# Kernel tuning notes

Hardware: AMD Instinct MI355X
Metric: run time of the kernel (lower is better)

Reference implementation:

```python
import jax, jax.numpy as jnp
import numpy as np

B, L1, LQ, LA, H = 32, 512, 32, 32, 128  # dialog turns, doc len, q len, a len, hidden
NEG = -1e30  # finite stand-in for torch's -inf (avoids NaN for fully-masked row 0, which is dropped by zero_first anyway)


def setup_inputs() -> dict:
    key = jax.random.key(0)
    ks = jax.random.split(key, 6)
    return {
        "xd_emb": jax.random.normal(ks[0], (B, L1, H), jnp.float32),
        "xq_emb": jax.random.normal(ks[1], (B, LQ, H), jnp.float32),
        "xa_emb": jax.random.normal(ks[2], (B, LA, H), jnp.float32),
        "W": jax.random.normal(ks[3], (H, H), jnp.float32) / np.sqrt(H).astype(np.float32),
        "b": jnp.zeros((H,), jnp.float32),
        "recency_weight": jnp.full((1,), -0.5, jnp.float32),
        "xq_mask": jax.random.randint(ks[4], (B, LQ), 0, 2).astype(bool),
        "xa_mask": jax.random.randint(ks[5], (B, LA), 0, 2).astype(bool),
    }


def _forward(xd_emb, xq_emb, xa_emb, W, b, recency_weight, xq_mask, xa_mask):
    Bn = xq_emb.shape[0]
    M = xq_emb.shape[1] + xa_emb.shape[1]  # max_dialog_len (max_qa_len)
    dlg = jnp.concatenate([xq_emb, xa_emb], axis=1).reshape(Bn * M, -1)  # (B*M, h) flattened dialog
    pad_mask = jnp.concatenate([xq_mask, xa_mask], axis=1).reshape(-1)    # (B*M,)

    ts = jnp.arange(Bn)
    j_ts = jnp.arange(Bn * M) // M  # timestep of each flattened dialog token
    # triu(ones, k=0) repeated M times along cols: timestep i masks tokens of timesteps >= i
    causal = j_ts[None, :] >= ts[:, None]            # (B, B*M)
    y_mask = causal | pad_mask[None, :]              # (B, B*M), True = masked

    # Linear + ReLU projections; y_proj computed once (no explicit (B, B*M, h) tiling)
    x_proj = jax.nn.relu(xd_emb @ W.T + b)           # (B, L1, h)
    y_proj = jax.nn.relu(dlg @ W.T + b)              # (B*M, h)

    scores = jnp.einsum('bld,kd->blk', x_proj, y_proj)      # (B, L1, B*M)
    scores = jnp.where(y_mask[:, None, :], jnp.float32(NEG), scores)

    # toeplitz recency bias: |i - j_ts| * recency_weight, row 0 zeroed (zero_first)
    rw = recency_weight[0] * jnp.abs(ts[:, None] - j_ts[None, :]).astype(jnp.float32)
    rw = jnp.concatenate([jnp.zeros_like(rw[:1]), rw[1:]], axis=0)
    scores = scores + rw[:, None, :]

    alpha = jax.nn.softmax(scores, axis=-1)
    alpha = jnp.concatenate([jnp.zeros_like(alpha[:1]), alpha[1:]], axis=0)  # zero_first
    return jnp.einsum('blk,kd->bld', alpha, dlg)     # weighted sum over original (unprojected) dialog


def reference(xd_emb, xq_emb, xa_emb, W, b, recency_weight, xq_mask, xa_mask):
    return _forward(xd_emb, xq_emb, xa_emb, W, b, recency_weight, xq_mask, xa_mask)
```

## Files before the change

### kernel.cpp

```cpp
#include <hip/hip_runtime.h>
#include <stdint.h>

#define NEGV (-1e30f)

constexpr int L1_ = 512;
constexpr int H_  = 128;
constexpr int NK_ = 2048;

typedef __attribute__((ext_vector_type(8))) _Float16 f16x8;
typedef __attribute__((ext_vector_type(2))) __fp16   h16x2;
typedef __attribute__((ext_vector_type(4))) float    f32x4;

static __device__ __forceinline__ uint16_t f2h(float x) {
    union { _Float16 h; uint16_t u; } cv; cv.h = (_Float16)x; return cv.u;
}


__global__ __launch_bounds__(256) void preproc_kernel(
        const float* __restrict__ xq,
        const float* __restrict__ xa,
        const float* __restrict__ W,
        const float* __restrict__ bias,
        const uint8_t* __restrict__ qm,
        const uint8_t* __restrict__ am,
        uint8_t* __restrict__ Y2,
        uint8_t* __restrict__ V2,
        uint8_t* __restrict__ W2,
        float* __restrict__ badd) {
    int b = blockIdx.x;
    int tid = threadIdx.x;
    __shared__ __align__(16) float sbuf[64 * 128];

    if (b < 128) {
        int k0 = b * 16;
        f32x4* xr4 = (f32x4*)sbuf;
#pragma unroll
        for (int i = 0; i < 2; ++i) {
            int idx = tid + i * 256;
            int row = idx >> 5, d4 = idx & 31;
            int k = k0 + row;
            int b2 = k >> 6, r = k & 63;
            const float* src = (r < 32) ? (xq + (size_t)(b2 * 32 + r) * H_)
                                        : (xa + (size_t)(b2 * 32 + (r - 32)) * H_);
            xr4[idx] = *(const f32x4*)(src + d4 * 4);
        }
        __syncthreads();
        int c = tid & 127, rh = tid >> 7;
        float acc[8];
#pragma unroll
        for (int i = 0; i < 8; ++i) acc[i] = 0.0f;
        const f32x4* w4 = (const f32x4*)(W + (size_t)c * H_);
        for (int d4 = 0; d4 < 32; ++d4) {
            f32x4 wv = w4[d4];
#pragma unroll
            for (int i = 0; i < 8; ++i) {
                f32x4 x = xr4[(rh * 8 + i) * 32 + d4];
                acc[i] += wv[0]*x[0] + wv[1]*x[1] + wv[2]*x[2] + wv[3]*x[3];
            }
        }
        float bc = bias[c];
        float* res = sbuf + 2048;
#pragma unroll
        for (int i = 0; i < 8; ++i)
            res[(rh * 8 + i) * H_ + c] = fmaxf(acc[i] + bc, 0.0f);
        __syncthreads();
        int ks = tid >> 6, l = tid & 63, n16 = l & 15, g = l >> 4;
        uint16_t hbuf[8];
#pragma unroll
        for (int j = 0; j < 8; ++j)
            hbuf[j] = f2h(res[n16 * H_ + ks * 32 + g * 8 + j]);
        uint8_t* dst = Y2 + (((size_t)b * 4 + ks) << 10) + l * 16;
        *(uint64_t*)dst       = ((const uint64_t*)hbuf)[0];
        *(uint64_t*)(dst + 8) = ((const uint64_t*)hbuf)[1];
    } else if (b < 160) {
        int kt = b - 128;
        f32x4* ld4 = (f32x4*)sbuf;
#pragma unroll
        for (int i = 0; i < 8; ++i) {
            int idx = tid + i * 256;
            int row = idx >> 5, d4 = idx & 31;
            const float* src = (row < 32) ? (xq + (size_t)(kt * 32 + row) * H_)
                                          : (xa + (size_t)(kt * 32 + row - 32) * H_);
            ld4[idx] = *(const f32x4*)(src + d4 * 4);
        }
        __syncthreads();
#pragma unroll
        for (int i = 0; i < 4; ++i) {
            int id = tid + i * 256;
            int cT = id >> 7, ks = (id >> 6) & 1, l = id & 63;
            int n16 = l & 15, g = l >> 4;
            uint16_t hbuf[8];
#pragma unroll
            for (int j = 0; j < 8; ++j)
                hbuf[j] = f2h(sbuf[(ks * 32 + g * 8 + j) * H_ + cT * 16 + n16]);
            uint8_t* dst = V2 + (((size_t)kt * 16 + cT * 2 + ks) << 10) + l * 16;
            *(uint64_t*)dst       = ((const uint64_t*)hbuf)[0];
            *(uint64_t*)(dst + 8) = ((const uint64_t*)hbuf)[1];
        }
    } else if (b == 160) {
        int* flags = (int*)sbuf;
        if (tid == 0) { flags[0] = 0; flags[1] = 0; }
        __syncthreads();
        uint32_t v = ((const uint32_t*)qm)[tid] | ((const uint32_t*)am)[tid];
        if (v & 0xFFu)        atomicOr(&flags[0], 1);
        if (v & 0xFFFFFF00u)  atomicOr(&flags[1], 1);
        __syncthreads();
        int f0 = flags[0], f1 = flags[1];
        int mode = (f0 && !f1) ? 0 : ((!f0 && f1) ? 1 : 2);
        for (int k = tid; k < NK_; k += 256) {
            int b2 = k >> 6, r = k & 63;
            int idx = b2 * 32 + (r < 32 ? r : r - 32);
            const uint8_t* src = (r < 32) ? qm : am;
            int p;
            if (mode == 0)      p = (((const int*)src)[idx] != 0);
            else if (mode == 1) p = (((const float*)src)[idx] != 0.0f);
            else                p = (src[idx] != 0);
            badd[k] = p ? NEGV : 0.0f;
        }
    } else {
        for (int h = 0; h < 2; ++h) {
            f32x4* s4 = (f32x4*)sbuf;
#pragma unroll
            for (int i = 0; i < 8; ++i) {
                int idx = tid + i * 256;
                s4[idx] = *(const f32x4*)(W + (size_t)h * 64 * H_ + idx * 4);
            }
            __syncthreads();
#pragma unroll
            for (int i = 0; i < 4; ++i) {
                int id = tid + i * 256;
                int ct = id >> 8, ks = (id >> 6) & 3, l = id & 63;
                int n16 = l & 15, g = l >> 4;
                uint16_t hb[8];
#pragma unroll
                for (int j = 0; j < 8; ++j)
                    hb[j] = f2h(sbuf[(ct * 16 + n16) * H_ + ks * 32 + g * 8 + j]);
                uint8_t* dst = W2 + (((size_t)((h * 4 + ct) * 4 + ks)) << 10) + l * 16;
                *(uint64_t*)dst       = ((const uint64_t*)hb)[0];
                *(uint64_t*)(dst + 8) = ((const uint64_t*)hb)[1];
            }
            __syncthreads();
        }
    }
}

__global__ __launch_bounds__(256, 2) void attn_kernel(
        const float*   __restrict__ xd,
        const uint8_t* __restrict__ W2,
        const float*   __restrict__ bias,
        const uint8_t* __restrict__ Y2,
        const uint8_t* __restrict__ V2,
        const float*   __restrict__ badd,
        const float*   __restrict__ rw,
        float* __restrict__ out) {
    int bid = blockIdx.x;
    int t, lt;
    if (bid < 256) { int p = bid >> 4; t = (p < 15) ? 31 - p : 16; lt = bid & 15; }
    else           { int b2 = bid - 256; int p = b2 >> 4; t = (p < 15) ? p + 1 : 0; lt = b2 & 15; }
    int l0 = lt << 5;
    int tid = threadIdx.x;

    __shared__ __align__(16) float smem[4 * 64 * 64];
    __shared__ float stats_m[4][32];
    __shared__ float stats_l[4][32];

    if (t == 0) {
        f32x4 z = {0.f, 0.f, 0.f, 0.f};
        f32x4* o4 = (f32x4*)(out + (size_t)l0 * H_);
        for (int i = tid; i < 32 * H_ / 4; i += 256) o4[i] = z;
        return;
    }

    int w = tid >> 6, lane = tid & 63, n16 = lane & 15, g = lane >> 4;
    int prow0 = n16, prow1 = 16 + n16;
    int swzP = (n16 & 7) << 4;

    uint16_t* xbuf  = (uint16_t*)((char*)smem + 16384);
    uint16_t* xpbuf = (uint16_t*)((char*)smem + 24576);
    {
        const float* xsrc = xd + (size_t)(t * L1_ + l0) * H_;
#pragma unroll
        for (int i = 0; i < 4; ++i) {
            int idx = tid + i * 256;
            int row = idx >> 5, c4 = idx & 31;
            f32x4 v = *(const f32x4*)(xsrc + idx * 4);
            uint16_t hb[4] = { f2h(v[0]), f2h(v[1]), f2h(v[2]), f2h(v[3]) };
            *(uint64_t*)((char*)xbuf + row * 256 + ((c4 * 8) ^ ((row & 7) << 4)))
                = *(const uint64_t*)hb;
        }
    }
    __syncthreads();
    {
        f16x8 af[2][4];
#pragma unroll
        for (int rT = 0; rT < 2; ++rT) {
            int row = rT * 16 + n16, swz = (row & 7) << 4;
#pragma unroll
            for (int ks = 0; ks < 4; ++ks)
                af[rT][ks] = *(const f16x8*)((char*)xbuf + row * 256 + ((ks * 64 + g * 16) ^ swz));
        }
        int cTa = 2 * w, cTb = 2 * w + 1;
        f32x4 z4 = {0.f, 0.f, 0.f, 0.f};
        f32x4 d00 = z4, d01 = z4, d10 = z4, d11 = z4;
#pragma unroll
        for (int ks = 0; ks < 4; ++ks) {
            f16x8 wfa = *(const f16x8*)(W2 + (((size_t)cTa * 4 + ks) << 10) + lane * 16);
            f16x8 wfb = *(const f16x8*)(W2 + (((size_t)cTb * 4 + ks) << 10) + lane * 16);
            d00 = __builtin_amdgcn_mfma_f32_16x16x32_f16(af[0][ks], wfa, d00, 0, 0, 0);
            d10 = __builtin_amdgcn_mfma_f32_16x16x32_f16(af[1][ks], wfa, d10, 0, 0, 0);
            d01 = __builtin_amdgcn_mfma_f32_16x16x32_f16(af[0][ks], wfb, d01, 0, 0, 0);
            d11 = __builtin_amdgcn_mfma_f32_16x16x32_f16(af[1][ks], wfb, d11, 0, 0, 0);
        }
        float bba = bias[cTa * 16 + n16], bbb = bias[cTb * 16 + n16];
#pragma unroll
        for (int rT = 0; rT < 2; ++rT) {
            const f32x4& da = rT ? d10 : d00;
            const f32x4& db = rT ? d11 : d01;
#pragma unroll
            for (int q = 0; q < 4; ++q) {
                int row = rT * 16 + g * 4 + q, swz = (row & 7) << 4;
                *(uint16_t*)((char*)xpbuf + row * 256 + (((cTa * 16 + n16) * 2) ^ swz))
                    = f2h(fmaxf(da[q] + bba, 0.0f));
                *(uint16_t*)((char*)xpbuf + row * 256 + (((cTb * 16 + n16) * 2) ^ swz))
                    = f2h(fmaxf(db[q] + bbb, 0.0f));
            }
        }
    }
    __syncthreads();
    f16x8 xf[2][4];
#pragma unroll
    for (int rT = 0; rT < 2; ++rT) {
        int row = rT * 16 + n16, swz = (row & 7) << 4;
#pragma unroll
        for (int ks = 0; ks < 4; ++ks)
            xf[rT][ks] = *(const f16x8*)((char*)xpbuf + row * 256 + ((ks * 64 + g * 16) ^ swz));
    }

    f32x4 zero4 = {0.f, 0.f, 0.f, 0.f};
    f32x4 acc[2][8];
#pragma unroll
    for (int a = 0; a < 2; ++a)
#pragma unroll
        for (int c = 0; c < 8; ++c) acc[a][c] = zero4;

    float m_r[2] = {-INFINITY, -INFINITY};
    float l_r[2] = {0.0f, 0.0f};
    float rww = rw[0];

    char* Pw = (char*)smem + w * 4096;

    for (int kt = w; kt < t; kt += 4) {
        const uint8_t* ybase = Y2 + ((size_t)kt << 14) + lane * 16;
        const uint8_t* vbase = V2 + ((size_t)kt << 14) + lane * 16;

        f16x8 yf[4][4];
#pragma unroll
        for (int kkT = 0; kkT < 4; ++kkT)
#pragma unroll
            for (int ks = 0; ks < 4; ++ks)
                yf[kkT][ks] = *(const f16x8*)(ybase + ((kkT * 4 + ks) << 10));
        f16x8 vbA[4][2];
#pragma unroll
        for (int cT = 0; cT < 4; ++cT) {
            vbA[cT][0] = *(const f16x8*)(vbase + ((cT * 2) << 10));
            vbA[cT][1] = *(const f16x8*)(vbase + ((cT * 2 + 1) << 10));
        }
        f32x4 ba4[4];
#pragma unroll
        for (int kkT = 0; kkT < 4; ++kkT)
            ba4[kkT] = *(const f32x4*)(badd + kt * 64 + kkT * 16 + g * 4);
        __builtin_amdgcn_sched_barrier(0);

        f32x4 ss[4][2];
#pragma unroll
        for (int kkT = 0; kkT < 4; ++kkT) { ss[kkT][0] = zero4; ss[kkT][1] = zero4; }
#pragma unroll
        for (int ks = 0; ks < 4; ++ks)
#pragma unroll
            for (int kkT = 0; kkT < 4; ++kkT) {
                ss[kkT][0] = __builtin_amdgcn_mfma_f32_16x16x32_f16(yf[kkT][ks], xf[0][ks], ss[kkT][0], 0, 0, 0);
                ss[kkT][1] = __builtin_amdgcn_mfma_f32_16x16x32_f16(yf[kkT][ks], xf[1][ks], ss[kkT][1], 0, 0, 0);
            }

        f16x8 vbB[4][2];
#pragma unroll
        for (int cT = 0; cT < 4; ++cT) {
            vbB[cT][0] = *(const f16x8*)(vbase + (((cT + 4) * 2) << 10));
            vbB[cT][1] = *(const f16x8*)(vbase + (((cT + 4) * 2 + 1) << 10));
        }
        __builtin_amdgcn_sched_barrier(0);

        float biasK = rww * (float)(t - kt);
#pragma unroll
        for (int kkT = 0; kkT < 4; ++kkT) {
            f32x4 ba = ba4[kkT] + biasK;
            ss[kkT][0] += ba;
            ss[kkT][1] += ba;
        }

        float sc[2];
#pragma unroll
        for (int rT = 0; rT < 2; ++rT) {
            f32x4 mx4 = ss[0][rT];
#pragma unroll
            for (int kkT = 1; kkT < 4; ++kkT) {
                mx4[0] = fmaxf(mx4[0], ss[kkT][rT][0]);
                mx4[1] = fmaxf(mx4[1], ss[kkT][rT][1]);
                mx4[2] = fmaxf(mx4[2], ss[kkT][rT][2]);
                mx4[3] = fmaxf(mx4[3], ss[kkT][rT][3]);
            }
            float mx = fmaxf(fmaxf(mx4[0], mx4[1]), fmaxf(mx4[2], mx4[3]));
            mx = fmaxf(mx, __shfl_xor(mx, 16));
            mx = fmaxf(mx, __shfl_xor(mx, 32));
            float mn = fmaxf(m_r[rT], mx);
            sc[rT] = __expf(m_r[rT] - mn);
            m_r[rT] = mn;
        }

#pragma unroll
        for (int rT = 0; rT < 2; ++rT) {
            int r = rT ? prow1 : prow0;
            float mn = m_r[rT];
            float ps = 0.0f;
#pragma unroll
            for (int kkT = 0; kkT < 4; ++kkT) {
                f32x4 p;
#pragma unroll
                for (int q = 0; q < 4; ++q) p[q] = __expf(ss[kkT][rT][q] - mn);
                ps += (p[0] + p[1]) + (p[2] + p[3]);
                union { h16x2 h2[2]; uint64_t u64; } pk;
                pk.h2[0] = __builtin_amdgcn_cvt_pkrtz(p[0], p[1]);
                pk.h2[1] = __builtin_amdgcn_cvt_pkrtz(p[2], p[3]);
                *(uint64_t*)(Pw + r * 128 + ((kkT * 32 + g * 8) ^ swzP)) = pk.u64;
            }
            ps += __shfl_xor(ps, 16);
            ps += __shfl_xor(ps, 32);
            l_r[rT] = l_r[rT] * sc[rT] + ps;
        }

        asm volatile("s_waitcnt lgkmcnt(0)" ::: "memory");

        if (!__all((sc[0] == 1.0f) && (sc[1] == 1.0f))) {
#pragma unroll
            for (int rT = 0; rT < 2; ++rT) {
                f32x4 s4;
#pragma unroll
                for (int q = 0; q < 4; ++q) s4[q] = __shfl(sc[rT], (g << 2) + q);
#pragma unroll
                for (int cT = 0; cT < 8; ++cT) acc[rT][cT] *= s4;
            }
        }

        f16x8 pa[2][2];
#pragma unroll
        for (int rT = 0; rT < 2; ++rT) {
            int r = rT ? prow1 : prow0;
#pragma unroll
            for (int ks = 0; ks < 2; ++ks)
                pa[rT][ks] = *(const f16x8*)(Pw + r * 128 + ((ks * 64 + g * 16) ^ swzP));
        }
#pragma unroll
        for (int cT = 0; cT < 4; ++cT)
#pragma unroll
            for (int rT = 0; rT < 2; ++rT) {
                acc[rT][cT] = __builtin_amdgcn_mfma_f32_16x16x32_f16(pa[rT][0], vbA[cT][0], acc[rT][cT], 0, 0, 0);
                acc[rT][cT] = __builtin_amdgcn_mfma_f32_16x16x32_f16(pa[rT][1], vbA[cT][1], acc[rT][cT], 0, 0, 0);
            }
#pragma unroll
        for (int cT = 0; cT < 4; ++cT)
#pragma unroll
            for (int rT = 0; rT < 2; ++rT) {
                acc[rT][cT + 4] = __builtin_amdgcn_mfma_f32_16x16x32_f16(pa[rT][0], vbB[cT][0], acc[rT][cT + 4], 0, 0, 0);
                acc[rT][cT + 4] = __builtin_amdgcn_mfma_f32_16x16x32_f16(pa[rT][1], vbB[cT][1], acc[rT][cT + 4], 0, 0, 0);
            }
    }

    if (g == 0) {
        stats_m[w][n16]      = m_r[0];
        stats_m[w][16 + n16] = m_r[1];
        stats_l[w][n16]      = l_r[0];
        stats_l[w][16 + n16] = l_r[1];
    }
    __syncthreads();

    float fac[2][4];
#pragma unroll
    for (int rT = 0; rT < 2; ++rT)
#pragma unroll
        for (int q = 0; q < 4; ++q) {
            int r = rT * 16 + (g << 2) + q;
            float m0 = stats_m[0][r], m1 = stats_m[1][r];
            float m2 = stats_m[2][r], m3 = stats_m[3][r];
            float mf = fmaxf(fmaxf(m0, m1), fmaxf(m2, m3));
            float lf = stats_l[0][r] * __expf(m0 - mf) + stats_l[1][r] * __expf(m1 - mf)
                     + stats_l[2][r] * __expf(m2 - mf) + stats_l[3][r] * __expf(m3 - mf);
            float mw = stats_m[w][r];
            fac[rT][q] = __expf(mw - mf) / lf;
        }

    float* Ob = smem + w * 4096;
#pragma unroll
    for (int rT = 0; rT < 2; ++rT)
#pragma unroll
        for (int cT = 0; cT < 8; ++cT)
#pragma unroll
            for (int q = 0; q < 4; ++q)
                Ob[((rT * 8 + cT) * 4 + q) * 64 + lane] = acc[rT][cT][q] * fac[rT][q];
    __syncthreads();

    size_t obase = (size_t)(t * L1_ + l0) * H_;
#pragma unroll
    for (int s = 0; s < 16; ++s) {
        int slot = w * 16 + s;
        float v = smem[slot * 64 + lane] + smem[4096 + slot * 64 + lane]
                + smem[8192 + slot * 64 + lane] + smem[12288 + slot * 64 + lane];
        int rT = slot >> 5, cT = (slot >> 2) & 7, q = slot & 3;
        out[obase + (size_t)(rT * 16 + (g << 2) + q) * H_ + cT * 16 + n16] = v;
    }
}

extern "C" void kernel_launch(void* const* d_in, const int* in_sizes, int n_in,
                              void* d_out, int out_size, void* d_ws, size_t ws_size,
                              hipStream_t stream) {
    const float*   xd   = (const float*)d_in[0];
    const float*   xq   = (const float*)d_in[1];
    const float*   xa   = (const float*)d_in[2];
    const float*   W    = (const float*)d_in[3];
    const float*   bias = (const float*)d_in[4];
    const float*   rw   = (const float*)d_in[5];
    const uint8_t* qm   = (const uint8_t*)d_in[6];
    const uint8_t* am   = (const uint8_t*)d_in[7];
    float* out = (float*)d_out;

    char* ws = (char*)d_ws;
    float*   badd = (float*)ws;
    uint8_t* Y2   = (uint8_t*)(ws + 8192);
    uint8_t* V2   = (uint8_t*)(ws + 8192 + 524288);
    uint8_t* W2   = (uint8_t*)(ws + 8192 + 2 * 524288);

    preproc_kernel<<<162, 256, 0, stream>>>(xq, xa, W, bias, qm, am,
                                            Y2, V2, W2, badd);
    attn_kernel<<<512, 256, 0, stream>>>(xd, W2, bias, Y2, V2, badd, rw, out);
}
```

Before: 37.14 us.

## Use eight waves per attention block to split key tiles finer

Doubles the attention block from 256 to 512 threads, so eight waves split the key-timestep loop instead of four. Each wave now computes one 16-column slice of the x projection. The cross-wave softmax merge and output reduction cover eight partials, done in two passes over row tiles to fit shared memory. This shortens the serial loop per wave for long timesteps, at the cost of more shared memory, an extra barrier and a larger reduction.

```diff
diff --git a/kernel.cpp b/kernel.cpp
--- a/kernel.cpp
+++ b/kernel.cpp
@@ -144,7 +144,7 @@
     }
 }
 
-__global__ __launch_bounds__(256, 2) void attn_kernel(
+__global__ __launch_bounds__(512, 2) void attn_kernel(
         const float*   __restrict__ xd,
         const uint8_t* __restrict__ W2,
         const float*   __restrict__ bias,
@@ -160,14 +160,14 @@
     int l0 = lt << 5;
     int tid = threadIdx.x;
 
-    __shared__ __align__(16) float smem[4 * 64 * 64];
-    __shared__ float stats_m[4][32];
-    __shared__ float stats_l[4][32];
+    __shared__ __align__(16) float smem[16384];
+    __shared__ float stats_m[8][32];
+    __shared__ float stats_l[8][32];
 
     if (t == 0) {
         f32x4 z = {0.f, 0.f, 0.f, 0.f};
         f32x4* o4 = (f32x4*)(out + (size_t)l0 * H_);
-        for (int i = tid; i < 32 * H_ / 4; i += 256) o4[i] = z;
+        for (int i = tid; i < 32 * H_ / 4; i += 512) o4[i] = z;
         return;
     }
 
@@ -175,13 +175,13 @@
     int prow0 = n16, prow1 = 16 + n16;
     int swzP = (n16 & 7) << 4;
 
-    uint16_t* xbuf  = (uint16_t*)((char*)smem + 16384);
-    uint16_t* xpbuf = (uint16_t*)((char*)smem + 24576);
+    uint16_t* xbuf  = (uint16_t*)((char*)smem + 32768);
+    uint16_t* xpbuf = (uint16_t*)((char*)smem + 40960);
     {
         const float* xsrc = xd + (size_t)(t * L1_ + l0) * H_;
 #pragma unroll
-        for (int i = 0; i < 4; ++i) {
-            int idx = tid + i * 256;
+        for (int i = 0; i < 2; ++i) {
+            int idx = tid + i * 512;
             int row = idx >> 5, c4 = idx & 31;
             f32x4 v = *(const f32x4*)(xsrc + idx * 4);
             uint16_t hb[4] = { f2h(v[0]), f2h(v[1]), f2h(v[2]), f2h(v[3]) };
@@ -199,30 +199,23 @@
             for (int ks = 0; ks < 4; ++ks)
                 af[rT][ks] = *(const f16x8*)((char*)xbuf + row * 256 + ((ks * 64 + g * 16) ^ swz));
         }
-        int cTa = 2 * w, cTb = 2 * w + 1;
         f32x4 z4 = {0.f, 0.f, 0.f, 0.f};
-        f32x4 d00 = z4, d01 = z4, d10 = z4, d11 = z4;
+        f32x4 d0 = z4, d1 = z4;
 #pragma unroll
         for (int ks = 0; ks < 4; ++ks) {
-            f16x8 wfa = *(const f16x8*)(W2 + (((size_t)cTa * 4 + ks) << 10) + lane * 16);
-            f16x8 wfb = *(const f16x8*)(W2 + (((size_t)cTb * 4 + ks) << 10) + lane * 16);
-            d00 = __builtin_amdgcn_mfma_f32_16x16x32_f16(af[0][ks], wfa, d00, 0, 0, 0);
-            d10 = __builtin_amdgcn_mfma_f32_16x16x32_f16(af[1][ks], wfa, d10, 0, 0, 0);
-            d01 = __builtin_amdgcn_mfma_f32_16x16x32_f16(af[0][ks], wfb, d01, 0, 0, 0);
-            d11 = __builtin_amdgcn_mfma_f32_16x16x32_f16(af[1][ks], wfb, d11, 0, 0, 0);
-        }
-        float bba = bias[cTa * 16 + n16], bbb = bias[cTb * 16 + n16];
+            f16x8 wf = *(const f16x8*)(W2 + (((size_t)w * 4 + ks) << 10) + lane * 16);
+            d0 = __builtin_amdgcn_mfma_f32_16x16x32_f16(af[0][ks], wf, d0, 0, 0, 0);
+            d1 = __builtin_amdgcn_mfma_f32_16x16x32_f16(af[1][ks], wf, d1, 0, 0, 0);
+        }
+        float bb = bias[w * 16 + n16];
 #pragma unroll
         for (int rT = 0; rT < 2; ++rT) {
-            const f32x4& da = rT ? d10 : d00;
-            const f32x4& db = rT ? d11 : d01;
+            const f32x4& d = rT ? d1 : d0;
 #pragma unroll
             for (int q = 0; q < 4; ++q) {
                 int row = rT * 16 + g * 4 + q, swz = (row & 7) << 4;
-                *(uint16_t*)((char*)xpbuf + row * 256 + (((cTa * 16 + n16) * 2) ^ swz))
-                    = f2h(fmaxf(da[q] + bba, 0.0f));
-                *(uint16_t*)((char*)xpbuf + row * 256 + (((cTb * 16 + n16) * 2) ^ swz))
-                    = f2h(fmaxf(db[q] + bbb, 0.0f));
+                *(uint16_t*)((char*)xpbuf + row * 256 + (((w * 16 + n16) * 2) ^ swz))
+                    = f2h(fmaxf(d[q] + bb, 0.0f));
             }
         }
     }
@@ -249,7 +242,7 @@
 
     char* Pw = (char*)smem + w * 4096;
 
-    for (int kt = w; kt < t; kt += 4) {
+    for (int kt = w; kt < t; kt += 8) {
         const uint8_t* ybase = Y2 + ((size_t)kt << 14) + lane * 16;
         const uint8_t* vbase = V2 + ((size_t)kt << 14) + lane * 16;
 
@@ -389,33 +382,34 @@
 #pragma unroll
         for (int q = 0; q < 4; ++q) {
             int r = rT * 16 + (g << 2) + q;
-            float m0 = stats_m[0][r], m1 = stats_m[1][r];
-            float m2 = stats_m[2][r], m3 = stats_m[3][r];
-            float mf = fmaxf(fmaxf(m0, m1), fmaxf(m2, m3));
-            float lf = stats_l[0][r] * __expf(m0 - mf) + stats_l[1][r] * __expf(m1 - mf)
-                     + stats_l[2][r] * __expf(m2 - mf) + stats_l[3][r] * __expf(m3 - mf);
-            float mw = stats_m[w][r];
-            fac[rT][q] = __expf(mw - mf) / lf;
-        }
-
-    float* Ob = smem + w * 4096;
-#pragma unroll
-    for (int rT = 0; rT < 2; ++rT)
+            float mf = stats_m[0][r];
+#pragma unroll
+            for (int wv = 1; wv < 8; ++wv) mf = fmaxf(mf, stats_m[wv][r]);
+            float lf = 0.0f;
+#pragma unroll
+            for (int wv = 0; wv < 8; ++wv) lf += stats_l[wv][r] * __expf(stats_m[wv][r] - mf);
+            fac[rT][q] = __expf(stats_m[w][r] - mf) / lf;
+        }
+
+    size_t obase = (size_t)(t * L1_ + l0) * H_;
+    for (int rT = 0; rT < 2; ++rT) {
+        float* Ob = smem + w * 2048;
 #pragma unroll
         for (int cT = 0; cT < 8; ++cT)
 #pragma unroll
             for (int q = 0; q < 4; ++q)
-                Ob[((rT * 8 + cT) * 4 + q) * 64 + lane] = acc[rT][cT][q] * fac[rT][q];
-    __syncthreads();
-
-    size_t obase = (size_t)(t * L1_ + l0) * H_;
-#pragma unroll
-    for (int s = 0; s < 16; ++s) {
-        int slot = w * 16 + s;
-        float v = smem[slot * 64 + lane] + smem[4096 + slot * 64 + lane]
-                + smem[8192 + slot * 64 + lane] + smem[12288 + slot * 64 + lane];
-        int rT = slot >> 5, cT = (slot >> 2) & 7, q = slot & 3;
-        out[obase + (size_t)(rT * 16 + (g << 2) + q) * H_ + cT * 16 + n16] = v;
+                Ob[(cT * 4 + q) * 64 + lane] = acc[rT][cT][q] * fac[rT][q];
+        __syncthreads();
+#pragma unroll
+        for (int s = 0; s < 4; ++s) {
+            int slot = w * 4 + s;
+            float v = 0.0f;
+#pragma unroll
+            for (int wv = 0; wv < 8; ++wv) v += smem[wv * 2048 + slot * 64 + lane];
+            int cT = slot >> 2, q = slot & 3;
+            out[obase + (size_t)(rT * 16 + (g << 2) + q) * H_ + cT * 16 + n16] = v;
+        }
+        __syncthreads();
     }
 }
 
@@ -440,5 +434,5 @@
 
     preproc_kernel<<<162, 256, 0, stream>>>(xq, xa, W, bias, qm, am,
                                             Y2, V2, W2, badd);
-    attn_kernel<<<512, 256, 0, stream>>>(xd, W2, bias, Y2, V2, badd, rw, out);
+    attn_kernel<<<512, 512, 0, stream>>>(xd, W2, bias, Y2, V2, badd, rw, out);
 }
```

Result: slower. 44.40 us (+19.6%).

## Split attention over key range into two halves with separate combine kernel

Applied to the files above, without the earlier changes.

Each (timestep, L-tile) work item is split into two blocks that each cover half of the causal key-timestep range. Partial unnormalized outputs and per-row max/sum statistics go to workspace, and a new combine kernel merges them with a log-sum-exp rescale. The aim is more blocks and a better-balanced triangular workload. Occupancy is raised to 4 blocks per CU by streaming Y/V fragments inside the MFMA loops instead of preloading them, and setprio is added around the MFMA sections. The cost is an extra kernel launch, roughly 16MB of partial-output traffic through global memory, and x_proj fragments reloaded from LDS on every iteration.

```diff
diff --git a/kernel.cpp b/kernel.cpp
--- a/kernel.cpp
+++ b/kernel.cpp
@@ -1,5 +1,6 @@
 #include <hip/hip_runtime.h>
 #include <stdint.h>
+#include <math.h>
 
 #define NEGV (-1e30f)
 
@@ -144,7 +145,7 @@
     }
 }
 
-__global__ __launch_bounds__(256, 2) void attn_kernel(
+__global__ __launch_bounds__(256, 4) void attn_kernel(
         const float*   __restrict__ xd,
         const uint8_t* __restrict__ W2,
         const float*   __restrict__ bias,
@@ -152,31 +153,31 @@
         const uint8_t* __restrict__ V2,
         const float*   __restrict__ badd,
         const float*   __restrict__ rw,
-        float* __restrict__ out) {
+        float* __restrict__ Opart,
+        float* __restrict__ mstat,
+        float* __restrict__ lstat) {
     int bid = blockIdx.x;
-    int t, lt;
-    if (bid < 256) { int p = bid >> 4; t = (p < 15) ? 31 - p : 16; lt = bid & 15; }
-    else           { int b2 = bid - 256; int p = b2 >> 4; t = (p < 15) ? p + 1 : 0; lt = b2 & 15; }
-    int l0 = lt << 5;
+    int r8 = bid & 255, qq = bid >> 8;
+    int tt = r8 >> 4, l = r8 & 15;
+    int t = (qq & 1) ? tt : (31 - tt);
+    int h = qq >> 1;
+    if (t == 0) return;
+    int l0 = l << 5;
+    int lo = h ? ((t + 1) >> 1) : 0;
+    int hi = h ? t : ((t + 1) >> 1);
     int tid = threadIdx.x;
 
-    __shared__ __align__(16) float smem[4 * 64 * 64];
+    __shared__ __align__(16) char LDSA[32768];
     __shared__ float stats_m[4][32];
     __shared__ float stats_l[4][32];
-
-    if (t == 0) {
-        f32x4 z = {0.f, 0.f, 0.f, 0.f};
-        f32x4* o4 = (f32x4*)(out + (size_t)l0 * H_);
-        for (int i = tid; i < 32 * H_ / 4; i += 256) o4[i] = z;
-        return;
-    }
 
     int w = tid >> 6, lane = tid & 63, n16 = lane & 15, g = lane >> 4;
     int prow0 = n16, prow1 = 16 + n16;
     int swzP = (n16 & 7) << 4;
-
-    uint16_t* xbuf  = (uint16_t*)((char*)smem + 16384);
-    uint16_t* xpbuf = (uint16_t*)((char*)smem + 24576);
+    char* xpbuf = LDSA + 16384;
+    char* xbuf  = LDSA + 24576;
+    char* Pw    = LDSA + w * 4096;
+
     {
         const float* xsrc = xd + (size_t)(t * L1_ + l0) * H_;
 #pragma unroll
@@ -185,8 +186,7 @@
             int row = idx >> 5, c4 = idx & 31;
             f32x4 v = *(const f32x4*)(xsrc + idx * 4);
             uint16_t hb[4] = { f2h(v[0]), f2h(v[1]), f2h(v[2]), f2h(v[3]) };
-            *(uint64_t*)((char*)xbuf + row * 256 + ((c4 * 8) ^ ((row & 7) << 4)))
-                = *(const uint64_t*)hb;
+            *(uint64_t*)(xbuf + row * 256 + ((c4 * 8) ^ ((row & 7) << 4))) = *(const uint64_t*)hb;
         }
     }
     __syncthreads();
@@ -197,7 +197,7 @@
             int row = rT * 16 + n16, swz = (row & 7) << 4;
 #pragma unroll
             for (int ks = 0; ks < 4; ++ks)
-                af[rT][ks] = *(const f16x8*)((char*)xbuf + row * 256 + ((ks * 64 + g * 16) ^ swz));
+                af[rT][ks] = *(const f16x8*)(xbuf + row * 256 + ((ks * 64 + g * 16) ^ swz));
         }
         int cTa = 2 * w, cTb = 2 * w + 1;
         f32x4 z4 = {0.f, 0.f, 0.f, 0.f};
@@ -217,24 +217,14 @@
             const f32x4& da = rT ? d10 : d00;
             const f32x4& db = rT ? d11 : d01;
 #pragma unroll
-            for (int q = 0; q < 4; ++q) {
-                int row = rT * 16 + g * 4 + q, swz = (row & 7) << 4;
-                *(uint16_t*)((char*)xpbuf + row * 256 + (((cTa * 16 + n16) * 2) ^ swz))
-                    = f2h(fmaxf(da[q] + bba, 0.0f));
-                *(uint16_t*)((char*)xpbuf + row * 256 + (((cTb * 16 + n16) * 2) ^ swz))
-                    = f2h(fmaxf(db[q] + bbb, 0.0f));
+            for (int q2 = 0; q2 < 4; ++q2) {
+                int row = rT * 16 + g * 4 + q2, swz = (row & 7) << 4;
+                *(uint16_t*)(xpbuf + row * 256 + (((cTa * 16 + n16) * 2) ^ swz)) = f2h(fmaxf(da[q2] + bba, 0.0f));
+                *(uint16_t*)(xpbuf + row * 256 + (((cTb * 16 + n16) * 2) ^ swz)) = f2h(fmaxf(db[q2] + bbb, 0.0f));
             }
         }
     }
     __syncthreads();
-    f16x8 xf[2][4];
-#pragma unroll
-    for (int rT = 0; rT < 2; ++rT) {
-        int row = rT * 16 + n16, swz = (row & 7) << 4;
-#pragma unroll
-        for (int ks = 0; ks < 4; ++ks)
-            xf[rT][ks] = *(const f16x8*)((char*)xpbuf + row * 256 + ((ks * 64 + g * 16) ^ swz));
-    }
 
     f32x4 zero4 = {0.f, 0.f, 0.f, 0.f};
     f32x4 acc[2][8];
@@ -242,58 +232,46 @@
     for (int a = 0; a < 2; ++a)
 #pragma unroll
         for (int c = 0; c < 8; ++c) acc[a][c] = zero4;
-
     float m_r[2] = {-INFINITY, -INFINITY};
     float l_r[2] = {0.0f, 0.0f};
     float rww = rw[0];
 
-    char* Pw = (char*)smem + w * 4096;
-
-    for (int kt = w; kt < t; kt += 4) {
+    for (int kt = lo + w; kt < hi; kt += 4) {
         const uint8_t* ybase = Y2 + ((size_t)kt << 14) + lane * 16;
         const uint8_t* vbase = V2 + ((size_t)kt << 14) + lane * 16;
 
-        f16x8 yf[4][4];
-#pragma unroll
-        for (int kkT = 0; kkT < 4; ++kkT)
+        f16x8 xf[2][4];
+#pragma unroll
+        for (int rT = 0; rT < 2; ++rT) {
+            int row = rT * 16 + n16;
 #pragma unroll
             for (int ks = 0; ks < 4; ++ks)
-                yf[kkT][ks] = *(const f16x8*)(ybase + ((kkT * 4 + ks) << 10));
-        f16x8 vbA[4][2];
-#pragma unroll
-        for (int cT = 0; cT < 4; ++cT) {
-            vbA[cT][0] = *(const f16x8*)(vbase + ((cT * 2) << 10));
-            vbA[cT][1] = *(const f16x8*)(vbase + ((cT * 2 + 1) << 10));
-        }
-        f32x4 ba4[4];
-#pragma unroll
-        for (int kkT = 0; kkT < 4; ++kkT)
-            ba4[kkT] = *(const f32x4*)(badd + kt * 64 + kkT * 16 + g * 4);
-        __builtin_amdgcn_sched_barrier(0);
+                xf[rT][ks] = *(const f16x8*)(xpbuf + row * 256 + ((ks * 64 + g * 16) ^ swzP));
+        }
 
         f32x4 ss[4][2];
 #pragma unroll
         for (int kkT = 0; kkT < 4; ++kkT) { ss[kkT][0] = zero4; ss[kkT][1] = zero4; }
-#pragma unroll
-        for (int ks = 0; ks < 4; ++ks)
+        __builtin_amdgcn_s_setprio(1);
+#pragma unroll
+        for (int ks = 0; ks < 4; ++ks) {
+            f16x8 yf[4];
+#pragma unroll
+            for (int kkT = 0; kkT < 4; ++kkT)
+                yf[kkT] = *(const f16x8*)(ybase + ((kkT * 4 + ks) << 10));
 #pragma unroll
             for (int kkT = 0; kkT < 4; ++kkT) {
-                ss[kkT][0] = __builtin_amdgcn_mfma_f32_16x16x32_f16(yf[kkT][ks], xf[0][ks], ss[kkT][0], 0, 0, 0);
-                ss[kkT][1] = __builtin_amdgcn_mfma_f32_16x16x32_f16(yf[kkT][ks], xf[1][ks], ss[kkT][1], 0, 0, 0);
-            }
-
-        f16x8 vbB[4][2];
-#pragma unroll
-        for (int cT = 0; cT < 4; ++cT) {
-            vbB[cT][0] = *(const f16x8*)(vbase + (((cT + 4) * 2) << 10));
-            vbB[cT][1] = *(const f16x8*)(vbase + (((cT + 4) * 2 + 1) << 10));
-        }
-        __builtin_amdgcn_sched_barrier(0);
+                ss[kkT][0] = __builtin_amdgcn_mfma_f32_16x16x32_f16(yf[kkT], xf[0][ks], ss[kkT][0], 0, 0, 0);
+                ss[kkT][1] = __builtin_amdgcn_mfma_f32_16x16x32_f16(yf[kkT], xf[1][ks], ss[kkT][1], 0, 0, 0);
+            }
+        }
+        __builtin_amdgcn_s_setprio(0);
 
         float biasK = rww * (float)(t - kt);
 #pragma unroll
         for (int kkT = 0; kkT < 4; ++kkT) {
-            f32x4 ba = ba4[kkT] + biasK;
+            f32x4 ba = *(const f32x4*)(badd + kt * 64 + kkT * 16 + g * 4);
+            ba += biasK;
             ss[kkT][0] += ba;
             ss[kkT][1] += ba;
         }
@@ -319,19 +297,19 @@
 
 #pragma unroll
         for (int rT = 0; rT < 2; ++rT) {
-            int r = rT ? prow1 : prow0;
+            int rr = rT ? prow1 : prow0;
             float mn = m_r[rT];
             float ps = 0.0f;
 #pragma unroll
             for (int kkT = 0; kkT < 4; ++kkT) {
                 f32x4 p;
 #pragma unroll
-                for (int q = 0; q < 4; ++q) p[q] = __expf(ss[kkT][rT][q] - mn);
+                for (int q2 = 0; q2 < 4; ++q2) p[q2] = __expf(ss[kkT][rT][q2] - mn);
                 ps += (p[0] + p[1]) + (p[2] + p[3]);
                 union { h16x2 h2[2]; uint64_t u64; } pk;
                 pk.h2[0] = __builtin_amdgcn_cvt_pkrtz(p[0], p[1]);
                 pk.h2[1] = __builtin_amdgcn_cvt_pkrtz(p[2], p[3]);
-                *(uint64_t*)(Pw + r * 128 + ((kkT * 32 + g * 8) ^ swzP)) = pk.u64;
+                *(uint64_t*)(Pw + rr * 128 + ((kkT * 32 + g * 8) ^ swzP)) = pk.u64;
             }
             ps += __shfl_xor(ps, 16);
             ps += __shfl_xor(ps, 32);
@@ -345,7 +323,7 @@
             for (int rT = 0; rT < 2; ++rT) {
                 f32x4 s4;
 #pragma unroll
-                for (int q = 0; q < 4; ++q) s4[q] = __shfl(sc[rT], (g << 2) + q);
+                for (int q2 = 0; q2 < 4; ++q2) s4[q2] = __shfl(sc[rT], (g << 2) + q2);
 #pragma unroll
                 for (int cT = 0; cT < 8; ++cT) acc[rT][cT] *= s4;
             }
@@ -354,25 +332,23 @@
         f16x8 pa[2][2];
 #pragma unroll
         for (int rT = 0; rT < 2; ++rT) {
-            int r = rT ? prow1 : prow0;
+            int rr = rT ? prow1 : prow0;
 #pragma unroll
             for (int ks = 0; ks < 2; ++ks)
-                pa[rT][ks] = *(const f16x8*)(Pw + r * 128 + ((ks * 64 + g * 16) ^ swzP));
-        }
-#pragma unroll
-        for (int cT = 0; cT < 4; ++cT)
+                pa[rT][ks] = *(const f16x8*)(Pw + rr * 128 + ((ks * 64 + g * 16) ^ swzP));
+        }
+        __builtin_amdgcn_s_setprio(1);
+#pragma unroll
+        for (int cT = 0; cT < 8; ++cT) {
+            f16x8 vb0 = *(const f16x8*)(vbase + ((cT * 2) << 10));
+            f16x8 vb1 = *(const f16x8*)(vbase + ((cT * 2 + 1) << 10));
 #pragma unroll
             for (int rT = 0; rT < 2; ++rT) {
-                acc[rT][cT] = __builtin_amdgcn_mfma_f32_16x16x32_f16(pa[rT][0], vbA[cT][0], acc[rT][cT], 0, 0, 0);
-                acc[rT][cT] = __builtin_amdgcn_mfma_f32_16x16x32_f16(pa[rT][1], vbA[cT][1], acc[rT][cT], 0, 0, 0);
-            }
-#pragma unroll
-        for (int cT = 0; cT < 4; ++cT)
-#pragma unroll
-            for (int rT = 0; rT < 2; ++rT) {
-                acc[rT][cT + 4] = __builtin_amdgcn_mfma_f32_16x16x32_f16(pa[rT][0], vbB[cT][0], acc[rT][cT + 4], 0, 0, 0);
-                acc[rT][cT + 4] = __builtin_amdgcn_mfma_f32_16x16x32_f16(pa[rT][1], vbB[cT][1], acc[rT][cT + 4], 0, 0, 0);
-            }
+                acc[rT][cT] = __builtin_amdgcn_mfma_f32_16x16x32_f16(pa[rT][0], vb0, acc[rT][cT], 0, 0, 0);
+                acc[rT][cT] = __builtin_amdgcn_mfma_f32_16x16x32_f16(pa[rT][1], vb1, acc[rT][cT], 0, 0, 0);
+            }
+        }
+        __builtin_amdgcn_s_setprio(0);
     }
 
     if (g == 0) {
@@ -387,36 +363,90 @@
 #pragma unroll
     for (int rT = 0; rT < 2; ++rT)
 #pragma unroll
-        for (int q = 0; q < 4; ++q) {
-            int r = rT * 16 + (g << 2) + q;
-            float m0 = stats_m[0][r], m1 = stats_m[1][r];
-            float m2 = stats_m[2][r], m3 = stats_m[3][r];
-            float mf = fmaxf(fmaxf(m0, m1), fmaxf(m2, m3));
-            float lf = stats_l[0][r] * __expf(m0 - mf) + stats_l[1][r] * __expf(m1 - mf)
-                     + stats_l[2][r] * __expf(m2 - mf) + stats_l[3][r] * __expf(m3 - mf);
-            float mw = stats_m[w][r];
-            fac[rT][q] = __expf(mw - mf) / lf;
-        }
-
-    float* Ob = smem + w * 4096;
-#pragma unroll
-    for (int rT = 0; rT < 2; ++rT)
+        for (int q2 = 0; q2 < 4; ++q2) {
+            int rr = rT * 16 + (g << 2) + q2;
+            float mw = stats_m[w][rr];
+            float mf = stats_m[0][rr];
+#pragma unroll
+            for (int wv = 1; wv < 4; ++wv) mf = fmaxf(mf, stats_m[wv][rr]);
+            fac[rT][q2] = (mw == -INFINITY) ? 0.0f : __expf(mw - mf);
+        }
+
+    float* Ob = (float*)LDSA;
+    float* op = Opart + (size_t)bid * 4096;
+    for (int rT = 0; rT < 2; ++rT) {
 #pragma unroll
         for (int cT = 0; cT < 8; ++cT)
 #pragma unroll
-            for (int q = 0; q < 4; ++q)
-                Ob[((rT * 8 + cT) * 4 + q) * 64 + lane] = acc[rT][cT][q] * fac[rT][q];
+            for (int q2 = 0; q2 < 4; ++q2)
+                Ob[w * 2048 + (cT * 4 + q2) * 64 + lane] = acc[rT][cT][q2] * fac[rT][q2];
+        __syncthreads();
+#pragma unroll
+        for (int s = 0; s < 8; ++s) {
+            int slot = w * 8 + s;
+            float v = Ob[slot * 64 + lane] + Ob[2048 + slot * 64 + lane]
+                    + Ob[4096 + slot * 64 + lane] + Ob[6144 + slot * 64 + lane];
+            int cT = slot >> 2, q2 = slot & 3;
+            op[(size_t)(rT * 16 + (g << 2) + q2) * 128 + cT * 16 + n16] = v;
+        }
+        __syncthreads();
+    }
+
+    if (tid < 32) {
+        float mf = stats_m[0][tid];
+#pragma unroll
+        for (int wv = 1; wv < 4; ++wv) mf = fmaxf(mf, stats_m[wv][tid]);
+        float lf = 0.0f;
+#pragma unroll
+        for (int wv = 0; wv < 4; ++wv) {
+            float mw = stats_m[wv][tid];
+            lf += stats_l[wv][tid] * ((mw == -INFINITY) ? 0.0f : __expf(mw - mf));
+        }
+        mstat[bid * 32 + tid] = mf;
+        lstat[bid * 32 + tid] = lf;
+    }
+}
+
+__global__ __launch_bounds__(256) void combine_kernel(
+        const float* __restrict__ Opart,
+        const float* __restrict__ mstat,
+        const float* __restrict__ lstat,
+        float* __restrict__ out) {
+    int c = blockIdx.x;
+    int t = c >> 4, l = c & 15;
+    int tid = threadIdx.x;
+    float* obase = out + (size_t)(t * L1_ + l * 32) * H_;
+
+    if (t == 0) {
+        f32x4 z = {0.f, 0.f, 0.f, 0.f};
+        f32x4* o4 = (f32x4*)obase;
+        for (int i = tid; i < 32 * H_ / 4; i += 256) o4[i] = z;
+        return;
+    }
+
+    int j0 = (t >= 16) ? (((31 - t) << 4) | l) : (256 + ((t << 4) | l));
+    int j1 = j0 + 512;
+
+    __shared__ float E0[32], E1[32], Li[32];
+    if (tid < 32) {
+        float m0 = mstat[j0 * 32 + tid], m1 = mstat[j1 * 32 + tid];
+        float s0 = lstat[j0 * 32 + tid], s1 = lstat[j1 * 32 + tid];
+        float M = fmaxf(m0, m1);
+        float e0 = (m0 == -INFINITY) ? 0.0f : __expf(m0 - M);
+        float e1 = (m1 == -INFINITY) ? 0.0f : __expf(m1 - M);
+        float L = s0 * e0 + s1 * e1;
+        E0[tid] = e0; E1[tid] = e1; Li[tid] = 1.0f / L;
+    }
     __syncthreads();
 
-    size_t obase = (size_t)(t * L1_ + l0) * H_;
-#pragma unroll
-    for (int s = 0; s < 16; ++s) {
-        int slot = w * 16 + s;
-        float v = smem[slot * 64 + lane] + smem[4096 + slot * 64 + lane]
-                + smem[8192 + slot * 64 + lane] + smem[12288 + slot * 64 + lane];
-        int rT = slot >> 5, cT = (slot >> 2) & 7, q = slot & 3;
-        out[obase + (size_t)(rT * 16 + (g << 2) + q) * H_ + cT * 16 + n16] = v;
-    }
+    int rr = tid >> 3, cg = tid & 7;
+    const f32x4* p0 = (const f32x4*)(Opart + (size_t)j0 * 4096 + rr * 128 + cg * 16);
+    const f32x4* p1 = (const f32x4*)(Opart + (size_t)j1 * 4096 + rr * 128 + cg * 16);
+    f32x4* po = (f32x4*)(obase + (size_t)rr * 128 + cg * 16);
+    float e0 = E0[rr], e1 = E1[rr], li = Li[rr];
+#pragma unroll
+    for (int v = 0; v < 4; ++v)
+        po[v] = (p0[v] * e0 + p1[v] * e1) * li;
 }
 
 extern "C" void kernel_launch(void* const* d_in, const int* in_sizes, int n_in,
@@ -433,12 +463,17 @@
     float* out = (float*)d_out;
 
     char* ws = (char*)d_ws;
-    float*   badd = (float*)ws;
-    uint8_t* Y2   = (uint8_t*)(ws + 8192);
-    uint8_t* V2   = (uint8_t*)(ws + 8192 + 524288);
-    uint8_t* W2   = (uint8_t*)(ws + 8192 + 2 * 524288);
+    float*   badd  = (float*)ws;
+    uint8_t* Y2    = (uint8_t*)(ws + 8192);
+    uint8_t* V2    = (uint8_t*)(ws + 8192 + 524288);
+    uint8_t* W2    = (uint8_t*)(ws + 8192 + 2 * 524288);
+    float*   Opart = (float*)(ws + 2 * 1024 * 1024);
+    float*   mstat = (float*)(ws + 18 * 1024 * 1024);
+    float*   lstat = (float*)(ws + 18 * 1024 * 1024 + 131072);
 
     preproc_kernel<<<162, 256, 0, stream>>>(xq, xa, W, bias, qm, am,
                                             Y2, V2, W2, badd);
-    attn_kernel<<<512, 256, 0, stream>>>(xd, W2, bias, Y2, V2, badd, rw, out);
+    attn_kernel<<<1024, 256, 0, stream>>>(xd, W2, bias, Y2, V2, badd, rw,
+                                          Opart, mstat, lstat);
+    combine_kernel<<<512, 256, 0, stream>>>(Opart, mstat, lstat, out);
 }
```

Result: slower. 68.29 us (+83.9%).
